# Kernel tuning notes

Hardware: AMD Instinct MI355X
Metric: run time of the kernel (lower is better)

The kernel has to match this reference:

```python
import jax, jax.numpy as jnp
import numpy as np

B, C, N, M, K = 1, 64, 65536, 65536, 16
H, O = 64, 128  # mlp hidden, out_channels


def setup_inputs() -> dict:
    key = jax.random.key(0)
    ks = jax.random.split(key, 8)
    return {
        "x": jax.random.normal(ks[0], (B, C, N), dtype=jnp.float32),
        "pos": jax.random.normal(ks[1], (B, 3, N), dtype=jnp.float32),
        "support_points": jax.random.normal(ks[2], (B, 3, M), dtype=jnp.float32),
        "W1": jax.random.normal(ks[3], (H, C + 3), dtype=jnp.float32) * 0.05,
        "b1": jax.random.normal(ks[4], (H,), dtype=jnp.float32) * 0.05,
        "W2": jax.random.normal(ks[5], (O, H), dtype=jnp.float32) * 0.05,
        "b2": jax.random.normal(ks[6], (O,), dtype=jnp.float32) * 0.05,
        "indices": jax.random.randint(ks[7], (B, M, K), 0, N, dtype=jnp.int64),
    }


def _gather_points(t, indices):
    # t: [B, C, N], indices: [B, M, K] -> [B, C, M, K]
    b, c, n = t.shape
    m, k = indices.shape[1], indices.shape[2]
    idx = indices.reshape(b, 1, m * k)  # broadcasts over channel dim
    return jnp.take_along_axis(t, idx, axis=2).reshape(b, c, m, k)


def reference(x, pos, support_points, W1, b1, W2, b2, indices):
    # gather neighbor features and positions: [B, C, M, K], [B, 3, M, K]
    feats = _gather_points(x, indices)
    pts = _gather_points(pos, indices) - support_points[:, :, :, None]
    h = jnp.concatenate([feats, pts], axis=1)  # [B, C+3, M, K]
    # shared per-point MLP (1x1 Conv2d == channel contraction)
    h = jnp.einsum("oc,bcmk->bomk", W1, h) + b1[None, :, None, None]
    h = jax.nn.relu(h)
    h = jnp.einsum("oc,bcmk->bomk", W2, h) + b2[None, :, None, None]
    # max-pool over neighborhood K -> [B, O, M]
    return jnp.max(h, axis=3)
```

## Files before the change

### kernel.cpp

```cpp
#include <hip/hip_runtime.h>

#define NPTS 65536
#define MPTS 65536
#define FSTR 72

typedef __attribute__((ext_vector_type(8))) short bf16x8;
typedef __attribute__((ext_vector_type(4))) float f32x4;

__device__ __forceinline__ float bflo(unsigned int u){ union{unsigned int i; float f;} v; v.i = u<<16; return v.f; }
__device__ __forceinline__ float bfhi(unsigned int u){ union{unsigned int i; float f;} v; v.i = u & 0xffff0000u; return v.f; }
__device__ __forceinline__ unsigned short f2bf(float f){
  union{float f; unsigned int i;} v; v.f=f;
  unsigned int r = v.i + 0x7fffu + ((v.i>>16)&1u);
  return (unsigned short)(r>>16);
}

#define MFMA32(a,b,c) __builtin_amdgcn_mfma_f32_16x16x32_bf16((a),(b),(c),0,0,0)

__global__ __launch_bounds__(256) void pack_all(
    const float* __restrict__ x, const float* __restrict__ pos,
    const float* __restrict__ W1, const float* __restrict__ W2,
    unsigned short* __restrict__ P2,
    unsigned short* __restrict__ W1F,
    unsigned short* __restrict__ W2F) {
  __shared__ unsigned int tile[64 * 37];
  const int t = threadIdx.x;
  const int n0 = blockIdx.x * 64;
  const int p = t & 63, cq = t >> 6;
  const int n = n0 + p;
  #pragma unroll
  for (int jj = 0; jj < 8; ++jj) {
    const int c = cq * 16 + 2 * jj;
    const unsigned int lo = f2bf(x[(size_t)c * NPTS + n]);
    const unsigned int hi = f2bf(x[(size_t)(c + 1) * NPTS + n]);
    tile[p * 37 + cq * 8 + jj] = lo | (hi << 16);
  }
  if (cq == 0) {
    const unsigned int a = f2bf(pos[n]);
    const unsigned int b = f2bf(pos[NPTS + n]);
    const unsigned int cc = f2bf(pos[2 * NPTS + n]);
    tile[p * 37 + 32] = a | (b << 16);
    tile[p * 37 + 33] = cc;
    tile[p * 37 + 34] = 0u;
    tile[p * 37 + 35] = 0u;
  }
  __syncthreads();
  unsigned int* Pd = (unsigned int*)(P2 + (size_t)n0 * FSTR);
  #pragma unroll
  for (int i = 0; i < 9; ++i) {
    const int u = t + i * 256;
    const int nl = u / 36, d = u - nl * 36;
    Pd[u] = tile[nl * 37 + d];
  }
  const int wid = blockIdx.x * 256 + t;
  if (wid < 768) {
    const int f = wid >> 6, lane = wid & 63;
    const int q = lane >> 4, lr = lane & 15;
    if (f < 8) {
      const int kt = f >> 2, nt = f & 3;
      #pragma unroll
      for (int j = 0; j < 8; ++j)
        W1F[wid*8 + j] = f2bf(W1[(nt*16 + lr)*67 + kt*32 + q*8 + j]);
    } else {
      const int nt = f - 8;
      #pragma unroll
      for (int j = 0; j < 8; ++j) {
        const int c = 64 + q*4 + j;
        W1F[wid*8 + j] = (j < 4 && c < 67) ? f2bf(W1[(nt*16 + lr)*67 + c]) : (unsigned short)0;
      }
    }
  } else if (wid < 768 + 2048) {
    const int gg = wid - 768;
    const int g = gg >> 6, lane = gg & 63;
    const int q = lane >> 4, lr = lane & 15;
    const int nt = g >> 3, ot = g & 7;
    #pragma unroll
    for (int j = 0; j < 8; ++j)
      W2F[gg*8 + j] = (j < 4) ? f2bf(W2[(ot*16 + lr)*64 + nt*16 + q*4 + j]) : (unsigned short)0;
  }
}

__global__ __launch_bounds__(256, 4) void pointnet_mfma(
    const unsigned short* __restrict__ P2,
    const float* __restrict__ sup,
    const unsigned short* __restrict__ W1F,
    const float* __restrict__ b1,
    const unsigned short* __restrict__ W2F,
    const float* __restrict__ b2,
    const int* __restrict__ indices,
    float* __restrict__ out) {
  __shared__ __align__(16) unsigned short featB[256 * FSTR];

  const int t = threadIdx.x;
  const int m0 = blockIdx.x * 16;
  const int lane = t & 63, w = t >> 6, quad = lane >> 4, lr = lane & 15;

  {
    const int idx = indices[m0*16 + t];
    const uint4* src = (const uint4*)(P2 + (size_t)idx * FSTR);
    uint4 u[9];
    #pragma unroll
    for (int i = 0; i < 9; ++i) u[i] = src[i];
    const int mm = m0 + (t >> 4);
    const float s0 = sup[mm], s1 = sup[MPTS + mm], s2 = sup[2*MPTS + mm];
    const float p0 = bflo(u[8].x), p1 = bfhi(u[8].x), p2 = bflo(u[8].y);
    u[8].x = (unsigned int)f2bf(p0 - s0) | ((unsigned int)f2bf(p1 - s1) << 16);
    u[8].y = (unsigned int)f2bf(p2 - s2);
    u[8].z = 0u; u[8].w = 0u;
    uint4* dst = (uint4*)(featB + t * FSTR);
    #pragma unroll
    for (int i = 0; i < 9; ++i) dst[i] = u[i];
  }

  const f32x4 fz = {0.f, 0.f, 0.f, 0.f};
  f32x4 acc1[4][4];
  #pragma unroll
  for (int nt = 0; nt < 4; ++nt)
    #pragma unroll
    for (int pt = 0; pt < 4; ++pt) acc1[nt][pt] = fz;

  #pragma unroll
  for (int kt = 0; kt < 2; ++kt) {
    bf16x8 wa[4];
    #pragma unroll
    for (int nt = 0; nt < 4; ++nt)
      wa[nt] = ((const bf16x8*)W1F)[(kt*4 + nt)*64 + lane];
    bf16x8 bf[4];
    #pragma unroll
    for (int pt = 0; pt < 4; ++pt)
      bf[pt] = *(const bf16x8*)&featB[(w*64 + pt*16 + lr)*FSTR + kt*32 + quad*8];
    #pragma unroll
    for (int nt = 0; nt < 4; ++nt)
      #pragma unroll
      for (int pt = 0; pt < 4; ++pt)
        acc1[nt][pt] = MFMA32(wa[nt], bf[pt], acc1[nt][pt]);
  }
  {
    bf16x8 wa16[4];
    #pragma unroll
    for (int nt = 0; nt < 4; ++nt)
      wa16[nt] = ((const bf16x8*)W1F)[(8 + nt)*64 + lane];
    bf16x8 bt[4];
    #pragma unroll
    for (int pt = 0; pt < 4; ++pt) {
      const uint2 d = *(const uint2*)&featB[(w*64 + pt*16 + lr)*FSTR + 64 + (quad & 1)*4];
      union { unsigned int u[4]; bf16x8 v; } mk;
      mk.u[0] = d.x; mk.u[1] = d.y; mk.u[2] = 0u; mk.u[3] = 0u;
      bt[pt] = mk.v;
    }
    #pragma unroll
    for (int nt = 0; nt < 4; ++nt)
      #pragma unroll
      for (int pt = 0; pt < 4; ++pt)
        acc1[nt][pt] = MFMA32(wa16[nt], bt[pt], acc1[nt][pt]);
  }

  unsigned int dwpk[4][4][2];
  #pragma unroll
  for (int nt = 0; nt < 4; ++nt) {
    const float4 bb = *(const float4*)(b1 + nt*16 + quad*4);
    #pragma unroll
    for (int pt = 0; pt < 4; ++pt) {
      const float v0 = fmaxf(acc1[nt][pt][0] + bb.x, 0.f);
      const float v1 = fmaxf(acc1[nt][pt][1] + bb.y, 0.f);
      const float v2 = fmaxf(acc1[nt][pt][2] + bb.z, 0.f);
      const float v3 = fmaxf(acc1[nt][pt][3] + bb.w, 0.f);
      dwpk[nt][pt][0] = (unsigned int)f2bf(v0) | ((unsigned int)f2bf(v1) << 16);
      dwpk[nt][pt][1] = (unsigned int)f2bf(v2) | ((unsigned int)f2bf(v3) << 16);
    }
  }

  #pragma unroll
  for (int ot = 0; ot < 8; ++ot) {
    f32x4 a2[4];
    #pragma unroll
    for (int pt = 0; pt < 4; ++pt) a2[pt] = fz;
    #pragma unroll
    for (int nt = 0; nt < 4; ++nt) {
      const bf16x8 wb = ((const bf16x8*)W2F)[(nt*8 + ot)*64 + lane];
      #pragma unroll
      for (int pt = 0; pt < 4; ++pt) {
        union { unsigned int u[4]; bf16x8 v; } mk;
        mk.u[0] = dwpk[nt][pt][0]; mk.u[1] = dwpk[nt][pt][1];
        mk.u[2] = 0u; mk.u[3] = 0u;
        a2[pt] = MFMA32(mk.v, wb, a2[pt]);
      }
    }
    float vm[4];
    #pragma unroll
    for (int pt = 0; pt < 4; ++pt) {
      float v = fmaxf(fmaxf(a2[pt][0], a2[pt][1]), fmaxf(a2[pt][2], a2[pt][3]));
      v = fmaxf(v, __shfl_xor(v, 16));
      v = fmaxf(v, __shfl_xor(v, 32));
      vm[pt] = v;
    }
    const float vq = (quad & 1) ? ((quad & 2) ? vm[3] : vm[1])
                                : ((quad & 2) ? vm[2] : vm[0]);
    const int o = ot*16 + lr;
    out[(size_t)o * MPTS + m0 + w*4 + quad] = vq + b2[o];
  }
}

__global__ __launch_bounds__(256) void pointnet_fallback(
    const float* __restrict__ x, const float* __restrict__ pos,
    const float* __restrict__ sup,
    const float* __restrict__ W1, const float* __restrict__ b1,
    const float* __restrict__ W2, const float* __restrict__ b2,
    const int* __restrict__ indices, float* __restrict__ out) {
  __shared__ float sfeat[16][68];
  __shared__ float shid[16][64];
  __shared__ float smax[4][128];
  __shared__ int sidx[16];
  const int t = threadIdx.x;
  const int m = blockIdx.x;
  if (t < 16) sidx[t] = indices[m*16 + t];
  const float sup0 = sup[m], sup1 = sup[MPTS + m], sup2 = sup[2*MPTS + m];
  __syncthreads();
  for (int u = t; u < 16*17; u += 256) {
    const int k = u / 17, c4 = (u - k*17) * 4;
    const int idx = sidx[k];
    float4 wv;
    if (c4 < 64) {
      wv.x = x[(size_t)(c4+0)*NPTS + idx]; wv.y = x[(size_t)(c4+1)*NPTS + idx];
      wv.z = x[(size_t)(c4+2)*NPTS + idx]; wv.w = x[(size_t)(c4+3)*NPTS + idx];
    } else {
      wv.x = pos[idx] - sup0; wv.y = pos[NPTS + idx] - sup1;
      wv.z = pos[2*NPTS + idx] - sup2; wv.w = 0.f;
    }
    *(float4*)&sfeat[k][c4] = wv;
  }
  const int h = t & 63, kg = t >> 6;
  float w1r[68];
  #pragma unroll
  for (int c = 0; c < 67; ++c) w1r[c] = W1[h*67 + c];
  w1r[67] = 0.f;
  const float bias1 = b1[h];
  __syncthreads();
  #pragma unroll
  for (int j = 0; j < 4; ++j) {
    const int k = kg*4 + j;
    float a = bias1;
    const float4* rr = (const float4*)sfeat[k];
    #pragma unroll
    for (int qq = 0; qq < 17; ++qq) {
      const float4 v = rr[qq];
      a += w1r[qq*4+0]*v.x + w1r[qq*4+1]*v.y + w1r[qq*4+2]*v.z + w1r[qq*4+3]*v.w;
    }
    shid[k][h] = fmaxf(a, 0.f);
  }
  const int ow = t & 63;
  float w2a[64], w2b[64];
  #pragma unroll
  for (int hh = 0; hh < 64; ++hh) { w2a[hh] = W2[ow*64 + hh]; w2b[hh] = W2[(ow+64)*64 + hh]; }
  __syncthreads();
  float mxa = -3.0e38f, mxb = -3.0e38f;
  #pragma unroll
  for (int j = 0; j < 4; ++j) {
    const int k = kg*4 + j;
    const float4* hr = (const float4*)shid[k];
    float pa = 0.f, pb = 0.f;
    #pragma unroll
    for (int qq = 0; qq < 16; ++qq) {
      const float4 v = hr[qq];
      pa += w2a[qq*4+0]*v.x + w2a[qq*4+1]*v.y + w2a[qq*4+2]*v.z + w2a[qq*4+3]*v.w;
      pb += w2b[qq*4+0]*v.x + w2b[qq*4+1]*v.y + w2b[qq*4+2]*v.z + w2b[qq*4+3]*v.w;
    }
    mxa = fmaxf(mxa, pa); mxb = fmaxf(mxb, pb);
  }
  smax[kg][ow] = mxa; smax[kg][64 + ow] = mxb;
  __syncthreads();
  if (t < 128) {
    out[(size_t)t * MPTS + m] =
        fmaxf(fmaxf(smax[0][t], smax[1][t]), fmaxf(smax[2][t], smax[3][t])) + b2[t];
  }
}

extern "C" void kernel_launch(void* const* d_in, const int* in_sizes, int n_in,
                              void* d_out, int out_size, void* d_ws, size_t ws_size,
                              hipStream_t stream) {
  const float* x   = (const float*)d_in[0];
  const float* pos = (const float*)d_in[1];
  const float* sup = (const float*)d_in[2];
  const float* W1  = (const float*)d_in[3];
  const float* b1  = (const float*)d_in[4];
  const float* W2  = (const float*)d_in[5];
  const float* b2  = (const float*)d_in[6];
  const int* indices = (const int*)d_in[7];
  float* out = (float*)d_out;

  const size_t P2_BYTES  = (size_t)NPTS * FSTR * 2;
  const size_t W1F_BYTES = 12 * 64 * 8 * 2;
  const size_t W2F_BYTES = 32 * 64 * 8 * 2;
  if (ws_size >= P2_BYTES + W1F_BYTES + W2F_BYTES) {
    unsigned short* P2  = (unsigned short*)d_ws;
    unsigned short* W1F = (unsigned short*)((char*)d_ws + P2_BYTES);
    unsigned short* W2F = (unsigned short*)((char*)d_ws + P2_BYTES + W1F_BYTES);
    pack_all<<<NPTS/64, 256, 0, stream>>>(x, pos, W1, W2, P2, W1F, W2F);
    pointnet_mfma<<<MPTS/16, 256, 0, stream>>>(P2, sup, W1F, b1, W2F, b2, indices, out);
  } else {
    pointnet_fallback<<<MPTS, 256, 0, stream>>>(x, pos, sup, W1, b1, W2, b2, indices, out);
  }
}
```

Before: 155.7 us.

## Restage layer-1 activations through LDS to use full-K MFMA for layer 2

Layer 2 previously ran 16x16x32 MFMAs with half of each operand zero-padded, wasting half of every instruction. The ReLU outputs are now written back into the shared feature buffer, reloaded in the MFMA operand layout, and fed to two full-K MFMAs per output tile. W2 is repacked to match, which halves its size. The layer-1 tail reads a full 8-wide vector instead of a half-zeroed one, relying on the padding columns in the packed buffer being zero. This adds an LDS write/read round trip in place of the register-held values.

```diff
diff --git a/kernel.cpp b/kernel.cpp
--- a/kernel.cpp
+++ b/kernel.cpp
@@ -69,14 +69,14 @@
         W1F[wid*8 + j] = (j < 4 && c < 67) ? f2bf(W1[(nt*16 + lr)*67 + c]) : (unsigned short)0;
       }
     }
-  } else if (wid < 768 + 2048) {
+  } else if (wid < 768 + 1024) {
     const int gg = wid - 768;
     const int g = gg >> 6, lane = gg & 63;
     const int q = lane >> 4, lr = lane & 15;
-    const int nt = g >> 3, ot = g & 7;
+    const int kt = g >> 3, ot = g & 7;
     #pragma unroll
     for (int j = 0; j < 8; ++j)
-      W2F[gg*8 + j] = (j < 4) ? f2bf(W2[(ot*16 + lr)*64 + nt*16 + q*4 + j]) : (unsigned short)0;
+      W2F[gg*8 + j] = f2bf(W2[(ot*16 + lr)*64 + kt*32 + q*8 + j]);
   }
 }
 
@@ -125,15 +125,15 @@
     #pragma unroll
     for (int nt = 0; nt < 4; ++nt)
       wa[nt] = ((const bf16x8*)W1F)[(kt*4 + nt)*64 + lane];
-    bf16x8 bf[4];
+    bf16x8 bfv[4];
     #pragma unroll
     for (int pt = 0; pt < 4; ++pt)
-      bf[pt] = *(const bf16x8*)&featB[(w*64 + pt*16 + lr)*FSTR + kt*32 + quad*8];
+      bfv[pt] = *(const bf16x8*)&featB[(w*64 + pt*16 + lr)*FSTR + kt*32 + quad*8];
     #pragma unroll
     for (int nt = 0; nt < 4; ++nt)
       #pragma unroll
       for (int pt = 0; pt < 4; ++pt)
-        acc1[nt][pt] = MFMA32(wa[nt], bf[pt], acc1[nt][pt]);
+        acc1[nt][pt] = MFMA32(wa[nt], bfv[pt], acc1[nt][pt]);
   }
   {
     bf16x8 wa16[4];
@@ -142,12 +142,8 @@
       wa16[nt] = ((const bf16x8*)W1F)[(8 + nt)*64 + lane];
     bf16x8 bt[4];
     #pragma unroll
-    for (int pt = 0; pt < 4; ++pt) {
-      const uint2 d = *(const uint2*)&featB[(w*64 + pt*16 + lr)*FSTR + 64 + (quad & 1)*4];
-      union { unsigned int u[4]; bf16x8 v; } mk;
-      mk.u[0] = d.x; mk.u[1] = d.y; mk.u[2] = 0u; mk.u[3] = 0u;
-      bt[pt] = mk.v;
-    }
+    for (int pt = 0; pt < 4; ++pt)
+      bt[pt] = *(const bf16x8*)&featB[(w*64 + pt*16 + lr)*FSTR + 64];
     #pragma unroll
     for (int nt = 0; nt < 4; ++nt)
       #pragma unroll
@@ -155,7 +151,6 @@
         acc1[nt][pt] = MFMA32(wa16[nt], bt[pt], acc1[nt][pt]);
   }
 
-  unsigned int dwpk[4][4][2];
   #pragma unroll
   for (int nt = 0; nt < 4; ++nt) {
     const float4 bb = *(const float4*)(b1 + nt*16 + quad*4);
@@ -165,26 +160,29 @@
       const float v1 = fmaxf(acc1[nt][pt][1] + bb.y, 0.f);
       const float v2 = fmaxf(acc1[nt][pt][2] + bb.z, 0.f);
       const float v3 = fmaxf(acc1[nt][pt][3] + bb.w, 0.f);
-      dwpk[nt][pt][0] = (unsigned int)f2bf(v0) | ((unsigned int)f2bf(v1) << 16);
-      dwpk[nt][pt][1] = (unsigned int)f2bf(v2) | ((unsigned int)f2bf(v3) << 16);
-    }
-  }
+      uint2 d;
+      d.x = (unsigned int)f2bf(v0) | ((unsigned int)f2bf(v1) << 16);
+      d.y = (unsigned int)f2bf(v2) | ((unsigned int)f2bf(v3) << 16);
+      *(uint2*)&featB[(w*64 + pt*16 + lr)*FSTR + nt*16 + quad*4] = d;
+    }
+  }
+
+  bf16x8 ah[4][2];
+  #pragma unroll
+  for (int pt = 0; pt < 4; ++pt)
+    #pragma unroll
+    for (int kt = 0; kt < 2; ++kt)
+      ah[pt][kt] = *(const bf16x8*)&featB[(w*64 + pt*16 + lr)*FSTR + kt*32 + quad*8];
 
   #pragma unroll
   for (int ot = 0; ot < 8; ++ot) {
+    const bf16x8 wb0 = ((const bf16x8*)W2F)[(0*8 + ot)*64 + lane];
+    const bf16x8 wb1 = ((const bf16x8*)W2F)[(1*8 + ot)*64 + lane];
     f32x4 a2[4];
     #pragma unroll
-    for (int pt = 0; pt < 4; ++pt) a2[pt] = fz;
-    #pragma unroll
-    for (int nt = 0; nt < 4; ++nt) {
-      const bf16x8 wb = ((const bf16x8*)W2F)[(nt*8 + ot)*64 + lane];
-      #pragma unroll
-      for (int pt = 0; pt < 4; ++pt) {
-        union { unsigned int u[4]; bf16x8 v; } mk;
-        mk.u[0] = dwpk[nt][pt][0]; mk.u[1] = dwpk[nt][pt][1];
-        mk.u[2] = 0u; mk.u[3] = 0u;
-        a2[pt] = MFMA32(mk.v, wb, a2[pt]);
-      }
+    for (int pt = 0; pt < 4; ++pt) {
+      a2[pt] = MFMA32(ah[pt][0], wb0, fz);
+      a2[pt] = MFMA32(ah[pt][1], wb1, a2[pt]);
     }
     float vm[4];
     #pragma unroll
@@ -290,7 +288,7 @@
 
   const size_t P2_BYTES  = (size_t)NPTS * FSTR * 2;
   const size_t W1F_BYTES = 12 * 64 * 8 * 2;
-  const size_t W2F_BYTES = 32 * 64 * 8 * 2;
+  const size_t W2F_BYTES = 16 * 64 * 8 * 2;
   if (ws_size >= P2_BYTES + W1F_BYTES + W2F_BYTES) {
     unsigned short* P2  = (unsigned short*)d_ws;
     unsigned short* W1F = (unsigned short*)((char*)d_ws + P2_BYTES);
```

After: 147.4 us. 1.06x faster.
